# Kernel optimization log

Hardware: AMD Instinct MI355X
Metric: run time of the kernel (lower is better)

The kernel has to match this reference:

```python
import jax, jax.numpy as jnp
import numpy as np

B, L, Z, H = 8, 256, 16, 256


def setup_inputs() -> dict:
    key = jax.random.key(0)
    k1, k2, k3, k4 = jax.random.split(key, 4)
    start_logits = jax.random.normal(k1, (B, L, H), dtype=jnp.float32)
    end_logits = jax.random.normal(k2, (B, L, H), dtype=jnp.float32)
    cls_logits = jax.random.normal(k3, (B, Z, H), dtype=jnp.float32)
    # nn.init.normal_(std=0.1)
    weight_start_end = 0.1 * jax.random.normal(k4, (H, H, H), dtype=jnp.float32)
    return {
        "start_logits": start_logits,
        "end_logits": end_logits,
        "cls_logits": cls_logits,
        "weight_start_end": weight_start_end,
    }


def reference(start_logits, end_logits, cls_logits, weight_start_end):
    # start: [b,x,i], weight: [i,o,j], end: [b,y,j], cls: [b,z,o]
    # Stage 1a: contract i ->  [b,x,o,j]  (GEMM: (b*x, i) @ (i, o*j))
    sw = jnp.einsum('bxi,ioj->bxoj', start_logits, weight_start_end)
    # Stage 1b: contract j ->  [b,x,y,o]
    start_end = jnp.einsum('bxoj,byj->bxyo', sw, end_logits)
    # Stage 2: contract o ->  [b,x,y,z]
    span_logits = jnp.einsum('bxyo,bzo->bxyz', start_end, cls_logits)
    return span_logits
```

## Files before the change

kernel.cpp:

```cpp
#include <hip/hip_runtime.h>


typedef __attribute__((ext_vector_type(8))) short          bf16x8;
typedef __attribute__((ext_vector_type(8))) unsigned short u16x8;
typedef __attribute__((ext_vector_type(4))) unsigned short u16x4;
typedef __attribute__((ext_vector_type(4))) float          f32x4;

#define LDST 40

__device__ __forceinline__ unsigned short f2bf(float f) {
    unsigned u = __builtin_bit_cast(unsigned, f);
    u += 0x7fff + ((u >> 16) & 1);
    return (unsigned short)(u >> 16);
}

template<bool BB16>
__global__ __launch_bounds__(512, 4)
void gemm_trans(const float* __restrict__ Ab, const void* __restrict__ Bbv,
                unsigned short* __restrict__ Cb,
                int lda, int ldb, int ldc,
                long aBS, int aSh, long bBS, long cBS)
{
    __shared__ unsigned short As[2][128 * LDST];
    __shared__ unsigned short Bs[2][128 * LDST];

    const int tid  = threadIdx.x;
    const int bz   = blockIdx.z;
    const int row0 = blockIdx.y * 128;
    const int col0 = blockIdx.x * 128;

    const float*          Af = Ab + (long)(bz >> aSh) * aBS;
    const float*          Bf = (const float*)Bbv          + (long)bz * bBS;
    const unsigned short* Bh = (const unsigned short*)Bbv + (long)bz * bBS;
    unsigned short*       C  = Cb + (long)bz * cBS;

    const int ar  = tid >> 2;
    const int akc = tid & 3;
    const int kp  = (tid & 15) * 2;
    const int ng  = (tid >> 4) * 4;

    const int wid = tid >> 6, lane = tid & 63;
    const int wm = wid >> 1, wn = wid & 1;
    const int lr = lane & 15, lg = lane >> 4;

    f32x4 acc[2][4] = {};

    float4 aP[2][2];
    float4 bPf[2][2];
    u16x4  bPh[2][2];

    auto LOAD = [&](int set, int k0) {
        const float* p = Af + (long)(row0 + ar) * lda + k0 + akc * 8;
        aP[set][0] = *(const float4*)p;
        aP[set][1] = *(const float4*)(p + 4);
        if constexpr (!BB16) {
            const float* q = Bf + (long)(k0 + kp) * ldb + col0 + ng;
            bPf[set][0] = *(const float4*)q;
            bPf[set][1] = *(const float4*)(q + ldb);
        } else {
            const unsigned short* q = Bh + (long)(k0 + kp) * ldb + col0 + ng;
            bPh[set][0] = *(const u16x4*)q;
            bPh[set][1] = *(const u16x4*)(q + ldb);
        }
    };

    auto WRITE = [&](int set, int buf) {
        u16x8 w;
        const float* v = (const float*)&aP[set][0];
#pragma unroll
        for (int e = 0; e < 8; ++e) w[e] = f2bf(v[e]);
        *(u16x8*)(As[buf] + ar * LDST + akc * 8) = w;

#pragma unroll
        for (int e = 0; e < 4; ++e) {
            unsigned lo, hi;
            if constexpr (!BB16) {
                const float* v0 = (const float*)&bPf[set][0];
                const float* v1 = (const float*)&bPf[set][1];
                lo = f2bf(v0[e]); hi = f2bf(v1[e]);
            } else {
                lo = bPh[set][0][e]; hi = bPh[set][1][e];
            }
            *(unsigned*)(Bs[buf] + (ng + e) * LDST + kp) = lo | (hi << 16);
        }
    };

    auto COMPUTE = [&](int buf) {
        bf16x8 aF[2], bF[4];
#pragma unroll
        for (int fm = 0; fm < 2; ++fm)
            aF[fm] = *(const bf16x8*)&As[buf][(wm * 32 + fm * 16 + lr) * LDST + lg * 8];
#pragma unroll
        for (int fn = 0; fn < 4; ++fn)
            bF[fn] = *(const bf16x8*)&Bs[buf][(wn * 64 + fn * 16 + lr) * LDST + lg * 8];
#pragma unroll
        for (int fm = 0; fm < 2; ++fm)
#pragma unroll
            for (int fn = 0; fn < 4; ++fn)
                acc[fm][fn] = __builtin_amdgcn_mfma_f32_16x16x32_bf16(
                    aF[fm], bF[fn], acc[fm][fn], 0, 0, 0);
    };

    LOAD(0, 0);
    WRITE(0, 0);
    LOAD(1, 32);
#pragma unroll
    for (int s = 0; s < 8; ++s) {
        asm volatile("s_waitcnt lgkmcnt(0)" ::: "memory");
        __builtin_amdgcn_s_barrier();
        if (s < 6) LOAD(s & 1, (s + 2) * 32);
        COMPUTE(s & 1);
        if (s < 7) WRITE((s + 1) & 1, (s + 1) & 1);
    }

#pragma unroll
    for (int fm = 0; fm < 2; ++fm)
#pragma unroll
        for (int q = 0; q < 4; ++q) {
            const long row = row0 + wm * 32 + fm * 16 + lg * 4 + q;
#pragma unroll
            for (int fn = 0; fn < 4; ++fn) {
                const int col = col0 + wn * 64 + fn * 16 + lr;
                C[row * (long)ldc + col] = f2bf(acc[fm][fn][q]);
            }
        }
}

__global__ __launch_bounds__(256)
void fused_out(const unsigned short* __restrict__ endbf,
               const unsigned short* __restrict__ T,
               float* __restrict__ out)
{
    const int tid = threadIdx.x;
    const int b = blockIdx.x >> 8;
    const int x = blockIdx.x & 255;
    const int wid = tid >> 6, lane = tid & 63;
    const int lr = lane & 15, lg = lane >> 4;

    const unsigned short* Arow = endbf + (long)b * 65536;
    const unsigned short* Bcol = T + (long)(b * 16 + lr) * 65536 + x * 256;

    f32x4 acc[4] = {};
    u16x8 a[2][4], bb[2];

    auto LOADF = [&](int set, int k0) {
#pragma unroll
        for (int fm = 0; fm < 4; ++fm)
            a[set][fm] = *(const u16x8*)(Arow + (long)(wid * 64 + fm * 16 + lr) * 256 + k0 + lg * 8);
        bb[set] = *(const u16x8*)(Bcol + k0 + lg * 8);
    };

    LOADF(0, 0);
#pragma unroll
    for (int s = 0; s < 8; ++s) {
        if (s < 7) LOADF((s + 1) & 1, (s + 1) * 32);
#pragma unroll
        for (int fm = 0; fm < 4; ++fm)
            acc[fm] = __builtin_amdgcn_mfma_f32_16x16x32_bf16(
                __builtin_bit_cast(bf16x8, a[s & 1][fm]),
                __builtin_bit_cast(bf16x8, bb[s & 1]), acc[fm], 0, 0, 0);
    }

    float* op = out + (long)(b * 256 + x) * 4096;
#pragma unroll
    for (int fm = 0; fm < 4; ++fm)
#pragma unroll
        for (int q = 0; q < 4; ++q)
            op[(wid * 64 + fm * 16 + lg * 4 + q) * 16 + lr] = acc[fm][q];
}

__global__ __launch_bounds__(256)
void cvt_bf16(const float* __restrict__ in, unsigned short* __restrict__ out)
{
    const int i = (blockIdx.x * 256 + threadIdx.x) * 8;
    float4 v0 = *(const float4*)(in + i);
    float4 v1 = *(const float4*)(in + i + 4);
    const float* v = (const float*)&v0;
    u16x8 w;
#pragma unroll
    for (int e = 0; e < 4; ++e) w[e] = f2bf(v[e]);
    const float* u = (const float*)&v1;
#pragma unroll
    for (int e = 0; e < 4; ++e) w[4 + e] = f2bf(u[e]);
    *(u16x8*)(out + i) = w;
}

extern "C" void kernel_launch(void* const* d_in, const int* in_sizes, int n_in,
                              void* d_out, int out_size, void* d_ws, size_t ws_size,
                              hipStream_t stream)
{
    const float* start = (const float*)d_in[0];
    const float* endl  = (const float*)d_in[1];
    const float* cls   = (const float*)d_in[2];
    const float* W     = (const float*)d_in[3];
    float* out = (float*)d_out;

    char* ws = (char*)d_ws;
    unsigned short* Wc    = (unsigned short*)ws;
    unsigned short* T     = (unsigned short*)(ws + 16777216);
    unsigned short* endbf = (unsigned short*)(ws + 33554432);

    hipLaunchKernelGGL(cvt_bf16, dim3(256), dim3(256), 0, stream, endl, endbf);

    hipLaunchKernelGGL((gemm_trans<false>), dim3(2, 1, 256), dim3(512), 0, stream,
        cls, (const void*)W, Wc, 256, 256, 65536, 0L, 0, 65536L, 256L);

    hipLaunchKernelGGL((gemm_trans<true>), dim3(2, 2, 128), dim3(512), 0, stream,
        start, (const void*)Wc, T, 256, 256, 256, 65536L, 4, 65536L, 65536L);

    hipLaunchKernelGGL(fused_out, dim3(2048), dim3(256), 0, stream, endbf, T, out);
}
```

Before: 174.5 us.

## Reorder intermediate T layout, pre-convert start to bf16, process two x per block

Stage-2 GEMM now writes its output in a [b,x,z,o] layout so the final kernel reads contiguous rows per x instead of strided columns. The start logits are converted to bf16 in the same conversion kernel as end logits, so the second GEMM loads bf16 A tiles and skips per-tile conversion. The final kernel handles two x values per block, reusing the loaded end tiles across both and halving the grid, and raises wave priority around the MFMA loop. Scattered 2-byte stores in the GEMM epilogue with a 4096 stride may cost some write efficiency.

```diff
diff --git a/kernel.cpp b/kernel.cpp
--- a/kernel.cpp
+++ b/kernel.cpp
@@ -14,9 +14,9 @@
     return (unsigned short)(u >> 16);
 }
 
-template<bool BB16>
+template<bool AB16, bool BB16, bool T2OUT>
 __global__ __launch_bounds__(512, 4)
-void gemm_trans(const float* __restrict__ Ab, const void* __restrict__ Bbv,
+void gemm_trans(const void* __restrict__ Abv, const void* __restrict__ Bbv,
                 unsigned short* __restrict__ Cb,
                 int lda, int ldb, int ldc,
                 long aBS, int aSh, long bBS, long cBS)
@@ -29,10 +29,10 @@
     const int row0 = blockIdx.y * 128;
     const int col0 = blockIdx.x * 128;
 
-    const float*          Af = Ab + (long)(bz >> aSh) * aBS;
+    const float*          Af = (const float*)Abv          + (long)(bz >> aSh) * aBS;
+    const unsigned short* Ah = (const unsigned short*)Abv + (long)(bz >> aSh) * aBS;
     const float*          Bf = (const float*)Bbv          + (long)bz * bBS;
     const unsigned short* Bh = (const unsigned short*)Bbv + (long)bz * bBS;
-    unsigned short*       C  = Cb + (long)bz * cBS;
 
     const int ar  = tid >> 2;
     const int akc = tid & 3;
@@ -45,14 +45,17 @@
 
     f32x4 acc[2][4] = {};
 
-    float4 aP[2][2];
-    float4 bPf[2][2];
-    u16x4  bPh[2][2];
+    float4 aPf[2][2]; u16x8 aPh[2];
+    float4 bPf[2][2]; u16x4 bPh[2][2];
 
     auto LOAD = [&](int set, int k0) {
-        const float* p = Af + (long)(row0 + ar) * lda + k0 + akc * 8;
-        aP[set][0] = *(const float4*)p;
-        aP[set][1] = *(const float4*)(p + 4);
+        if constexpr (!AB16) {
+            const float* p = Af + (long)(row0 + ar) * lda + k0 + akc * 8;
+            aPf[set][0] = *(const float4*)p;
+            aPf[set][1] = *(const float4*)(p + 4);
+        } else {
+            aPh[set] = *(const u16x8*)(Ah + (long)(row0 + ar) * lda + k0 + akc * 8);
+        }
         if constexpr (!BB16) {
             const float* q = Bf + (long)(k0 + kp) * ldb + col0 + ng;
             bPf[set][0] = *(const float4*)q;
@@ -66,9 +69,13 @@
 
     auto WRITE = [&](int set, int buf) {
         u16x8 w;
-        const float* v = (const float*)&aP[set][0];
-#pragma unroll
-        for (int e = 0; e < 8; ++e) w[e] = f2bf(v[e]);
+        if constexpr (!AB16) {
+            const float* v = (const float*)&aPf[set][0];
+#pragma unroll
+            for (int e = 0; e < 8; ++e) w[e] = f2bf(v[e]);
+        } else {
+            w = aPh[set];
+        }
         *(u16x8*)(As[buf] + ar * LDST + akc * 8) = w;
 
 #pragma unroll
@@ -121,58 +128,80 @@
 #pragma unroll
             for (int fn = 0; fn < 4; ++fn) {
                 const int col = col0 + wn * 64 + fn * 16 + lr;
-                C[row * (long)ldc + col] = f2bf(acc[fm][fn][q]);
+                if constexpr (T2OUT) {
+                    unsigned short* Cq = Cb + (long)(bz >> 4) * 1048576 + (bz & 15) * 256;
+                    Cq[row * 4096 + col] = f2bf(acc[fm][fn][q]);
+                } else {
+                    unsigned short* Cq = Cb + (long)bz * cBS;
+                    Cq[row * (long)ldc + col] = f2bf(acc[fm][fn][q]);
+                }
             }
         }
 }
 
 __global__ __launch_bounds__(256)
 void fused_out(const unsigned short* __restrict__ endbf,
-               const unsigned short* __restrict__ T,
+               const unsigned short* __restrict__ T2,
                float* __restrict__ out)
 {
     const int tid = threadIdx.x;
-    const int b = blockIdx.x >> 8;
-    const int x = blockIdx.x & 255;
+    const int b  = blockIdx.x >> 7;
+    const int xp = blockIdx.x & 127;
     const int wid = tid >> 6, lane = tid & 63;
     const int lr = lane & 15, lg = lane >> 4;
 
     const unsigned short* Arow = endbf + (long)b * 65536;
-    const unsigned short* Bcol = T + (long)(b * 16 + lr) * 65536 + x * 256;
-
-    f32x4 acc[4] = {};
-    u16x8 a[2][4], bb[2];
+    const unsigned short* B0 = T2 + ((long)(b * 256 + xp * 2) * 16 + lr) * 256;
+    const unsigned short* B1 = B0 + 4096;
+
+    f32x4 acc0[4] = {}, acc1[4] = {};
+    u16x8 a[2][4], pb0[2], pb1[2];
 
     auto LOADF = [&](int set, int k0) {
 #pragma unroll
         for (int fm = 0; fm < 4; ++fm)
             a[set][fm] = *(const u16x8*)(Arow + (long)(wid * 64 + fm * 16 + lr) * 256 + k0 + lg * 8);
-        bb[set] = *(const u16x8*)(Bcol + k0 + lg * 8);
+        pb0[set] = *(const u16x8*)(B0 + k0 + lg * 8);
+        pb1[set] = *(const u16x8*)(B1 + k0 + lg * 8);
     };
 
     LOADF(0, 0);
 #pragma unroll
     for (int s = 0; s < 8; ++s) {
         if (s < 7) LOADF((s + 1) & 1, (s + 1) * 32);
-#pragma unroll
-        for (int fm = 0; fm < 4; ++fm)
-            acc[fm] = __builtin_amdgcn_mfma_f32_16x16x32_bf16(
+        __builtin_amdgcn_s_setprio(1);
+#pragma unroll
+        for (int fm = 0; fm < 4; ++fm) {
+            acc0[fm] = __builtin_amdgcn_mfma_f32_16x16x32_bf16(
                 __builtin_bit_cast(bf16x8, a[s & 1][fm]),
-                __builtin_bit_cast(bf16x8, bb[s & 1]), acc[fm], 0, 0, 0);
+                __builtin_bit_cast(bf16x8, pb0[s & 1]), acc0[fm], 0, 0, 0);
+            acc1[fm] = __builtin_amdgcn_mfma_f32_16x16x32_bf16(
+                __builtin_bit_cast(bf16x8, a[s & 1][fm]),
+                __builtin_bit_cast(bf16x8, pb1[s & 1]), acc1[fm], 0, 0, 0);
+        }
+        __builtin_amdgcn_s_setprio(0);
     }
 
-    float* op = out + (long)(b * 256 + x) * 4096;
+    float* op0 = out + (long)(b * 256 + xp * 2) * 4096;
+    float* op1 = op0 + 4096;
 #pragma unroll
     for (int fm = 0; fm < 4; ++fm)
 #pragma unroll
-        for (int q = 0; q < 4; ++q)
-            op[(wid * 64 + fm * 16 + lg * 4 + q) * 16 + lr] = acc[fm][q];
+        for (int q = 0; q < 4; ++q) {
+            const int y = wid * 64 + fm * 16 + lg * 4 + q;
+            op0[y * 16 + lr] = acc0[fm][q];
+            op1[y * 16 + lr] = acc1[fm][q];
+        }
 }
 
 __global__ __launch_bounds__(256)
-void cvt_bf16(const float* __restrict__ in, unsigned short* __restrict__ out)
-{
-    const int i = (blockIdx.x * 256 + threadIdx.x) * 8;
+void cvt_bf16(const float* __restrict__ endl, const float* __restrict__ start,
+              unsigned short* __restrict__ endbf, unsigned short* __restrict__ startbf)
+{
+    const int which = blockIdx.x >> 8;
+    const float* in = which ? start : endl;
+    unsigned short* out = which ? startbf : endbf;
+    const int i = ((blockIdx.x & 255) * 256 + threadIdx.x) * 8;
     float4 v0 = *(const float4*)(in + i);
     float4 v1 = *(const float4*)(in + i + 4);
     const float* v = (const float*)&v0;
@@ -196,17 +225,19 @@
     float* out = (float*)d_out;
 
     char* ws = (char*)d_ws;
-    unsigned short* Wc    = (unsigned short*)ws;
-    unsigned short* T     = (unsigned short*)(ws + 16777216);
-    unsigned short* endbf = (unsigned short*)(ws + 33554432);
-
-    hipLaunchKernelGGL(cvt_bf16, dim3(256), dim3(256), 0, stream, endl, endbf);
-
-    hipLaunchKernelGGL((gemm_trans<false>), dim3(2, 1, 256), dim3(512), 0, stream,
-        cls, (const void*)W, Wc, 256, 256, 65536, 0L, 0, 65536L, 256L);
-
-    hipLaunchKernelGGL((gemm_trans<true>), dim3(2, 2, 128), dim3(512), 0, stream,
-        start, (const void*)Wc, T, 256, 256, 256, 65536L, 4, 65536L, 65536L);
-
-    hipLaunchKernelGGL(fused_out, dim3(2048), dim3(256), 0, stream, endbf, T, out);
-}
+    unsigned short* Wc      = (unsigned short*)ws;
+    unsigned short* T2      = (unsigned short*)(ws + 16777216);
+    unsigned short* endbf   = (unsigned short*)(ws + 33554432);
+    unsigned short* startbf = (unsigned short*)(ws + 34603008);
+
+    hipLaunchKernelGGL(cvt_bf16, dim3(512), dim3(256), 0, stream,
+        endl, start, endbf, startbf);
+
+    hipLaunchKernelGGL((gemm_trans<false, false, false>), dim3(2, 1, 256), dim3(512), 0, stream,
+        (const void*)cls, (const void*)W, Wc, 256, 256, 65536, 0L, 0, 65536L, 256L);
+
+    hipLaunchKernelGGL((gemm_trans<true, true, true>), dim3(2, 2, 128), dim3(512), 0, stream,
+        (const void*)startbf, (const void*)Wc, T2, 256, 256, 4096, 65536L, 4, 65536L, 0L);
+
+    hipLaunchKernelGGL(fused_out, dim3(1024), dim3(256), 0, stream, endbf, T2, out);
+}
```

Measured after the change: 158.6 us. -9.1%, faster.
